# Kernel tuning notes

Measured on AMD Instinct MI355X. Metric: run time of the kernel, lower is better.

Reference implementation:

```python
import jax, jax.numpy as jnp
import numpy as np

B, N, F, K = 512, 128, 128, 4


def setup_inputs() -> dict:
    key = jax.random.key(0)
    ks = jax.random.split(key, 12)
    # xavier-normal-ish scales
    s_rw = float(np.sqrt(2.0 / (F + F)))
    s_sw = float(np.sqrt(2.0 / (F + F)))
    inp = {
        "H": jax.random.normal(ks[0], (B, N, F), dtype=jnp.float32),
        "E": jax.random.uniform(ks[1], (B, N, N, K), dtype=jnp.float32),
        "RW1": jax.random.normal(ks[2], (F, F, K), dtype=jnp.float32) * s_rw,
        "SW1": jax.random.normal(ks[3], (F, F), dtype=jnp.float32) * s_sw,
        "RW2": jax.random.normal(ks[4], (F, F, K), dtype=jnp.float32) * s_rw,
        "SW2": jax.random.normal(ks[5], (F, F), dtype=jnp.float32) * s_sw,
        "RW3": jax.random.normal(ks[6], (F, F, K), dtype=jnp.float32) * s_rw,
        "SW3": jax.random.normal(ks[7], (F, F), dtype=jnp.float32) * s_sw,
        "W1": jax.random.normal(ks[8], (F, 20), dtype=jnp.float32) * float(np.sqrt(1.0 / F)),
        "b1": jnp.zeros((20,), dtype=jnp.float32),
        "W2": jax.random.normal(ks[9], (20, 1), dtype=jnp.float32) * float(np.sqrt(1.0 / 20)),
        "b2": jnp.zeros((1,), dtype=jnp.float32),
    }
    return inp


def _rgcn_conv(H, E, D, RW, SW):
    # einsum('bi,bijk,bjm,mnk->bin') done in two GEMM-shaped steps
    M = jnp.einsum('bijk,bjm->bimk', E, H)          # [B,N,F,K]
    msg = jnp.einsum('bimk,mnk->bin', M, RW)        # [B,N,F]
    return jax.nn.sigmoid(msg * D[:, :, None] + jnp.einsum('bij,jl->bil', H, SW))


def reference(H, E, RW1, SW1, RW2, SW2, RW3, SW3, W1, b1, W2, b2):
    # degree norm with self-loops: (E + eye)[b,i,:,:].sum() = E.sum((2,3)) + K
    k = jnp.asarray(E.shape[-1], dtype=E.dtype)
    D = 1.0 / (E.sum(axis=(2, 3)) + k)              # [B,N]
    H = _rgcn_conv(H, E, D, RW1, SW1)
    H = _rgcn_conv(H, E, D, RW2, SW2)
    H = _rgcn_conv(H, E, D, RW3, SW3)
    h = jnp.maximum(H @ W1 + b1, 0.1 * (H @ W1 + b1))  # LeakyReLU(0.1)
    score = jnp.mean(jax.nn.sigmoid(h @ W2 + b2))
    return score
```

## Files before the change

### kernel.cpp

```cpp
#include <hip/hip_runtime.h>
#include <math.h>

#define BB 512
#define NN 128
#define FF 128
#define KK 4

typedef __attribute__((ext_vector_type(8))) short bf16x8;
typedef __attribute__((ext_vector_type(4))) float f32x4;

__device__ inline unsigned short f2bf(float x) {
  union { float f; unsigned int u; } v; v.f = x;
  unsigned int r = v.u + 0x7fff + ((v.u >> 16) & 1);
  return (unsigned short)(r >> 16);
}
__device__ inline float bf2f(unsigned short h) {
  union { unsigned int u; float f; } v; v.u = ((unsigned int)h) << 16; return v.f;
}

__global__ __launch_bounds__(256) void k_convE(const float* __restrict__ E,
                                               unsigned short* __restrict__ Eb,
                                               float* __restrict__ Dv) {
  int wave = threadIdx.x >> 6;
  int lane = threadIdx.x & 63;
  int row  = blockIdx.x * 4 + wave;
  const float* p = E + (size_t)row * 512 + lane * 8;
  f32x4 a = *(const f32x4*)p;
  f32x4 b = *(const f32x4*)(p + 4);
  float s = a[0] + a[1] + a[2] + a[3] + b[0] + b[1] + b[2] + b[3];
  #pragma unroll
  for (int off = 32; off > 0; off >>= 1) s += __shfl_down(s, off, 64);
  if (lane == 0) Dv[row] = 1.0f / (s + 4.0f);
  union { unsigned short h[8]; f32x4 v; } u;
  u.h[0] = f2bf(a[0]); u.h[1] = f2bf(a[1]); u.h[2] = f2bf(a[2]); u.h[3] = f2bf(a[3]);
  u.h[4] = f2bf(b[0]); u.h[5] = f2bf(b[1]); u.h[6] = f2bf(b[2]); u.h[7] = f2bf(b[3]);
  *(f32x4*)(Eb + (size_t)row * 512 + lane * 8) = u.v;
}

__global__ __launch_bounds__(256) void k_convH(const float* __restrict__ H,
                                               unsigned short* __restrict__ Hb) {
  size_t i = ((size_t)blockIdx.x * 256 + threadIdx.x) * 8;
  f32x4 a = *(const f32x4*)(H + i);
  f32x4 b = *(const f32x4*)(H + i + 4);
  union { unsigned short h[8]; f32x4 v; } u;
  u.h[0] = f2bf(a[0]); u.h[1] = f2bf(a[1]); u.h[2] = f2bf(a[2]); u.h[3] = f2bf(a[3]);
  u.h[4] = f2bf(b[0]); u.h[5] = f2bf(b[1]); u.h[6] = f2bf(b[2]); u.h[7] = f2bf(b[3]);
  *(f32x4*)(Hb + i) = u.v;
}

__global__ __launch_bounds__(256) void k_buildW(const float* __restrict__ RW,
                                                const float* __restrict__ SW,
                                                unsigned short* __restrict__ W2) {
  int idx = blockIdx.x * 256 + threadIdx.x;
  int m = idx & 127;
  int c = idx >> 7;
  float v = (c < 512) ? RW[m * 512 + c] : SW[m * 128 + (c - 512)];
  W2[idx] = f2bf(v);
}

__global__ __launch_bounds__(256) void k_gemm_g(
    const unsigned short* __restrict__ Hb,
    const unsigned short* __restrict__ W2,
    unsigned short* __restrict__ Gt,
    float* __restrict__ St)
{
  const int cb = blockIdx.x;
  const int b  = blockIdx.y;
  const unsigned short* A  = Hb + (size_t)b * 16384;
  const unsigned short* Bm = W2 + cb * 128 * 128;

  __shared__ unsigned short As[128 * 40];
  __shared__ unsigned short Bs[128 * 40];

  const int tid = threadIdx.x;
  const int w = tid >> 6, l = tid & 63;
  const int wr = w >> 1, wc = w & 1;
  const int lq = l >> 4, lm = l & 15;

  const int srow = tid >> 1;
  const int sch  = (tid & 1) * 16;

  f32x4 acc[4][4] = {};

  for (int k0 = 0; k0 < 128; k0 += 32) {
    f32x4 va0 = *(const f32x4*)(A + srow * 128 + k0 + sch);
    f32x4 va1 = *(const f32x4*)(A + srow * 128 + k0 + sch + 8);
    f32x4 vb0 = *(const f32x4*)(Bm + srow * 128 + k0 + sch);
    f32x4 vb1 = *(const f32x4*)(Bm + srow * 128 + k0 + sch + 8);
    __syncthreads();
    *(f32x4*)(As + srow * 40 + sch)     = va0;
    *(f32x4*)(As + srow * 40 + sch + 8) = va1;
    *(f32x4*)(Bs + srow * 40 + sch)     = vb0;
    *(f32x4*)(Bs + srow * 40 + sch + 8) = vb1;
    __syncthreads();
    bf16x8 fa[4], fb[4];
    #pragma unroll
    for (int f = 0; f < 4; ++f)
      fa[f] = *(const bf16x8*)(As + (wr * 64 + f * 16 + lm) * 40 + lq * 8);
    #pragma unroll
    for (int g = 0; g < 4; ++g)
      fb[g] = *(const bf16x8*)(Bs + (wc * 64 + g * 16 + lm) * 40 + lq * 8);
    #pragma unroll
    for (int f = 0; f < 4; ++f)
      #pragma unroll
      for (int g = 0; g < 4; ++g)
        acc[f][g] = __builtin_amdgcn_mfma_f32_16x16x32_bf16(fa[f], fb[g], acc[f][g], 0, 0, 0);
  }

  const int cbase = cb * 128 + wc * 64;
  if (cb < 4) {
    unsigned short* gt = Gt + (size_t)b * 65536;
    #pragma unroll
    for (int g = 0; g < 4; ++g) {
      int c = cbase + g * 16 + lm;
      int n = c >> 2, kk = c & 3;
      #pragma unroll
      for (int f = 0; f < 4; ++f) {
        int j0 = wr * 64 + f * 16 + lq * 4;
        #pragma unroll
        for (int r = 0; r < 4; ++r)
          gt[n * 512 + (j0 + r) * 4 + kk] = f2bf(acc[f][g][r]);
      }
    }
  } else {
    float* st = St + (size_t)b * 16384;
    #pragma unroll
    for (int g = 0; g < 4; ++g) {
      int s = wc * 64 + g * 16 + lm;
      #pragma unroll
      for (int f = 0; f < 4; ++f) {
        int j0 = wr * 64 + f * 16 + lq * 4;
        *(f32x4*)(st + s * 128 + j0) = acc[f][g];
      }
    }
  }
}

__global__ __launch_bounds__(256) void k_gemm_e(
    const unsigned short* __restrict__ Eb,
    const unsigned short* __restrict__ Gt,
    const float* __restrict__ St,
    const float* __restrict__ Dv,
    unsigned short* __restrict__ Hout)
{
  const int b = blockIdx.x;
  const unsigned short* A  = Eb + (size_t)b * 65536;
  const unsigned short* Bm = Gt + (size_t)b * 65536;

  __shared__ unsigned short As[128 * 40];
  __shared__ unsigned short Bs[128 * 40];

  const int tid = threadIdx.x;
  const int w = tid >> 6, l = tid & 63;
  const int wr = w >> 1, wc = w & 1;
  const int lq = l >> 4, lm = l & 15;

  const int srow = tid >> 1;
  const int sch  = (tid & 1) * 16;

  f32x4 acc[4][4] = {};

  for (int k0 = 0; k0 < 512; k0 += 32) {
    f32x4 va0 = *(const f32x4*)(A + srow * 512 + k0 + sch);
    f32x4 va1 = *(const f32x4*)(A + srow * 512 + k0 + sch + 8);
    f32x4 vb0 = *(const f32x4*)(Bm + srow * 512 + k0 + sch);
    f32x4 vb1 = *(const f32x4*)(Bm + srow * 512 + k0 + sch + 8);
    __syncthreads();
    *(f32x4*)(As + srow * 40 + sch)     = va0;
    *(f32x4*)(As + srow * 40 + sch + 8) = va1;
    *(f32x4*)(Bs + srow * 40 + sch)     = vb0;
    *(f32x4*)(Bs + srow * 40 + sch + 8) = vb1;
    __syncthreads();
    bf16x8 fa[4], fb[4];
    #pragma unroll
    for (int f = 0; f < 4; ++f)
      fa[f] = *(const bf16x8*)(As + (wr * 64 + f * 16 + lm) * 40 + lq * 8);
    #pragma unroll
    for (int g = 0; g < 4; ++g)
      fb[g] = *(const bf16x8*)(Bs + (wc * 64 + g * 16 + lm) * 40 + lq * 8);
    #pragma unroll
    for (int f = 0; f < 4; ++f)
      #pragma unroll
      for (int g = 0; g < 4; ++g)
        acc[f][g] = __builtin_amdgcn_mfma_f32_16x16x32_bf16(fa[f], fb[g], acc[f][g], 0, 0, 0);
  }

  const float* st = St + (size_t)b * 16384;
  const float* dv = Dv + b * 128;
  unsigned short* ho = Hout + (size_t)b * 16384;
  #pragma unroll
  for (int f = 0; f < 4; ++f) {
    int i0 = wr * 64 + f * 16 + lq * 4;
    f32x4 d = *(const f32x4*)(dv + i0);
    #pragma unroll
    for (int g = 0; g < 4; ++g) {
      int n = wc * 64 + g * 16 + lm;
      f32x4 sv = *(const f32x4*)(st + n * 128 + i0);
      #pragma unroll
      for (int r = 0; r < 4; ++r) {
        float v = fmaf(acc[f][g][r], d[r], sv[r]);
        ho[(i0 + r) * 128 + n] = f2bf(1.0f / (1.0f + __expf(-v)));
      }
    }
  }
}

__global__ __launch_bounds__(256) void k_mlp(
    const unsigned short* __restrict__ H,
    const float* __restrict__ W1,
    const float* __restrict__ b1,
    const float* __restrict__ W2,
    const float* __restrict__ b2,
    float* __restrict__ sumOut)
{
  __shared__ float W1s[128 * 20];
  __shared__ float b1s[20], W2s[20];
  __shared__ float red[256];
  for (int i = threadIdx.x; i < 2560; i += 256) W1s[i] = W1[i];
  if (threadIdx.x < 20) { b1s[threadIdx.x] = b1[threadIdx.x]; W2s[threadIdx.x] = W2[threadIdx.x]; }
  __syncthreads();

  int row = blockIdx.x * 256 + threadIdx.x;
  float h[20];
  #pragma unroll
  for (int j = 0; j < 20; ++j) h[j] = b1s[j];
  const unsigned short* hr = H + (size_t)row * 128;
  for (int m8 = 0; m8 < 128; m8 += 8) {
    f32x4 pk = *(const f32x4*)(hr + m8);
    const unsigned short* us = (const unsigned short*)&pk;
    #pragma unroll
    for (int e = 0; e < 8; ++e) {
      float x = bf2f(us[e]);
      #pragma unroll
      for (int j = 0; j < 20; ++j) h[j] = fmaf(x, W1s[(m8 + e) * 20 + j], h[j]);
    }
  }
  float v = b2[0];
  #pragma unroll
  for (int j = 0; j < 20; ++j) {
    float t = h[j];
    t = fmaxf(t, 0.1f * t);
    v = fmaf(t, W2s[j], v);
  }
  float s = 1.0f / (1.0f + __expf(-v));

  red[threadIdx.x] = s;
  __syncthreads();
  #pragma unroll
  for (int off = 128; off > 0; off >>= 1) {
    if (threadIdx.x < off) red[threadIdx.x] += red[threadIdx.x + off];
    __syncthreads();
  }
  if (threadIdx.x == 0) atomicAdd(sumOut, red[0]);
}

__global__ void k_final(const float* __restrict__ sum, float* __restrict__ out) {
  out[0] = sum[0] * (1.0f / 65536.0f);
}

extern "C" void kernel_launch(void* const* d_in, const int* in_sizes, int n_in,
                              void* d_out, int out_size, void* d_ws, size_t ws_size,
                              hipStream_t stream) {
  const float* H   = (const float*)d_in[0];
  const float* E   = (const float*)d_in[1];
  const float* RW1 = (const float*)d_in[2];
  const float* SW1 = (const float*)d_in[3];
  const float* RW2 = (const float*)d_in[4];
  const float* SW2 = (const float*)d_in[5];
  const float* RW3 = (const float*)d_in[6];
  const float* SW3 = (const float*)d_in[7];
  const float* W1  = (const float*)d_in[8];
  const float* b1  = (const float*)d_in[9];
  const float* W2  = (const float*)d_in[10];
  const float* b2  = (const float*)d_in[11];
  float* out = (float*)d_out;

  char* w = (char*)d_ws;
  float*          wsD   = (float*)w;                     w += 65536 * 4;
  unsigned short* wsEb  = (unsigned short*)w;            w += (size_t)33554432 * 2;
  unsigned short* wsGt  = (unsigned short*)w;            w += (size_t)33554432 * 2;
  float*          wsSt  = (float*)w;                     w += (size_t)8388608 * 4;
  unsigned short* wsHa  = (unsigned short*)w;            w += (size_t)8388608 * 2;
  unsigned short* wsHb  = (unsigned short*)w;            w += (size_t)8388608 * 2;
  unsigned short* wsW2  = (unsigned short*)w;            w += (size_t)3 * 81920 * 2;
  float*          wsSum = (float*)w;                     w += 256;

  k_convE<<<BB * NN / 4, 256, 0, stream>>>(E, wsEb, wsD);
  k_convH<<<8388608 / (256 * 8), 256, 0, stream>>>(H, wsHa);
  k_buildW<<<320, 256, 0, stream>>>(RW1, SW1, wsW2);
  k_buildW<<<320, 256, 0, stream>>>(RW2, SW2, wsW2 + 81920);
  k_buildW<<<320, 256, 0, stream>>>(RW3, SW3, wsW2 + 163840);
  hipMemsetAsync(wsSum, 0, sizeof(float), stream);

  k_gemm_g<<<dim3(5, BB), 256, 0, stream>>>(wsHa, wsW2, wsGt, wsSt);
  k_gemm_e<<<BB, 256, 0, stream>>>(wsEb, wsGt, wsSt, wsD, wsHb);
  k_gemm_g<<<dim3(5, BB), 256, 0, stream>>>(wsHb, wsW2 + 81920, wsGt, wsSt);
  k_gemm_e<<<BB, 256, 0, stream>>>(wsEb, wsGt, wsSt, wsD, wsHa);
  k_gemm_g<<<dim3(5, BB), 256, 0, stream>>>(wsHa, wsW2 + 163840, wsGt, wsSt);
  k_gemm_e<<<BB, 256, 0, stream>>>(wsEb, wsGt, wsSt, wsD, wsHb);

  k_mlp<<<BB * NN / 256, 256, 0, stream>>>(wsHb, W1, b1, W2, b2, wsSum);
  k_final<<<1, 1, 0, stream>>>(wsSum, out);
}
```

Before: 494.2 us.

## Fuse per-layer G and E GEMMs into one kernel keeping G in LDS

Each RGCN layer's two kernels (H·W into a global Gt/St buffer, then E·G with epilogue) become one kernel per batch. It builds the G tile in shared memory in two halves and computes the self-term GEMM in registers, so the 64 MB Gt and the St fp32 buffers never go through global memory. Operands now load straight from global into MFMA fragments without LDS staging. In exchange, W2 is re-read by every block, the grid shrinks to 512 blocks, and register pressure is high with three accumulator sets.

```diff
diff --git a/kernel.cpp b/kernel.cpp
--- a/kernel.cpp
+++ b/kernel.cpp
@@ -58,148 +58,112 @@
   W2[idx] = f2bf(v);
 }
 
-__global__ __launch_bounds__(256) void k_gemm_g(
-    const unsigned short* __restrict__ Hb,
-    const unsigned short* __restrict__ W2,
-    unsigned short* __restrict__ Gt,
-    float* __restrict__ St)
+#define GS_PITCH 264
+
+__global__ __launch_bounds__(256, 2) void k_layer(
+    const unsigned short* __restrict__ Eb,
+    const unsigned short* __restrict__ Hin,
+    const unsigned short* __restrict__ W2L,
+    const float* __restrict__ Dv,
+    unsigned short* __restrict__ Hout)
 {
-  const int cb = blockIdx.x;
-  const int b  = blockIdx.y;
-  const unsigned short* A  = Hb + (size_t)b * 16384;
-  const unsigned short* Bm = W2 + cb * 128 * 128;
-
-  __shared__ unsigned short As[128 * 40];
-  __shared__ unsigned short Bs[128 * 40];
+  __shared__ unsigned short Gs[128 * GS_PITCH];
+
+  const int b = blockIdx.x;
+  const unsigned short* E_b = Eb  + (size_t)b * 65536;
+  const unsigned short* H_b = Hin + (size_t)b * 16384;
 
   const int tid = threadIdx.x;
   const int w = tid >> 6, l = tid & 63;
   const int wr = w >> 1, wc = w & 1;
   const int lq = l >> 4, lm = l & 15;
 
-  const int srow = tid >> 1;
-  const int sch  = (tid & 1) * 16;
-
-  f32x4 acc[4][4] = {};
-
+  f32x4 macc[4][4] = {};
+
+  #pragma unroll
+  for (int h = 0; h < 2; ++h) {
+    __syncthreads();
+
+    #pragma unroll
+    for (int cb = 0; cb < 4; ++cb) {
+      f32x4 gacc[4][2] = {};
+      #pragma unroll
+      for (int k0 = 0; k0 < 128; k0 += 32) {
+        bf16x8 fa[4], fb[2];
+        #pragma unroll
+        for (int f = 0; f < 4; ++f)
+          fa[f] = *(const bf16x8*)(W2L + (cb * 128 + wr * 64 + f * 16 + lm) * 128 + k0 + lq * 8);
+        #pragma unroll
+        for (int g = 0; g < 2; ++g)
+          fb[g] = *(const bf16x8*)(H_b + (h * 64 + wc * 32 + g * 16 + lm) * 128 + k0 + lq * 8);
+        #pragma unroll
+        for (int f = 0; f < 4; ++f)
+          #pragma unroll
+          for (int g = 0; g < 2; ++g)
+            gacc[f][g] = __builtin_amdgcn_mfma_f32_16x16x32_bf16(fa[f], fb[g], gacc[f][g], 0, 0, 0);
+      }
+      #pragma unroll
+      for (int f = 0; f < 4; ++f) {
+        int n = cb * 32 + wr * 16 + f * 4 + lq;
+        #pragma unroll
+        for (int g = 0; g < 2; ++g) {
+          int jl = wc * 32 + g * 16 + lm;
+          union { unsigned short h4[4]; uint2 v; } u;
+          u.h4[0] = f2bf(gacc[f][g][0]); u.h4[1] = f2bf(gacc[f][g][1]);
+          u.h4[2] = f2bf(gacc[f][g][2]); u.h4[3] = f2bf(gacc[f][g][3]);
+          *(uint2*)(&Gs[n * GS_PITCH + jl * 4]) = u.v;
+        }
+      }
+    }
+    __syncthreads();
+
+    #pragma unroll
+    for (int kt = 0; kt < 8; ++kt) {
+      bf16x8 fa[4], fb[4];
+      #pragma unroll
+      for (int f = 0; f < 4; ++f)
+        fa[f] = *(const bf16x8*)(E_b + (wr * 64 + f * 16 + lm) * 512 + h * 256 + kt * 32 + lq * 8);
+      #pragma unroll
+      for (int g = 0; g < 4; ++g)
+        fb[g] = *(const bf16x8*)(&Gs[(wc * 64 + g * 16 + lm) * GS_PITCH + kt * 32 + lq * 8]);
+      #pragma unroll
+      for (int f = 0; f < 4; ++f)
+        #pragma unroll
+        for (int g = 0; g < 4; ++g)
+          macc[f][g] = __builtin_amdgcn_mfma_f32_16x16x32_bf16(fa[f], fb[g], macc[f][g], 0, 0, 0);
+    }
+  }
+
+  f32x4 sacc[4][4] = {};
+  #pragma unroll
   for (int k0 = 0; k0 < 128; k0 += 32) {
-    f32x4 va0 = *(const f32x4*)(A + srow * 128 + k0 + sch);
-    f32x4 va1 = *(const f32x4*)(A + srow * 128 + k0 + sch + 8);
-    f32x4 vb0 = *(const f32x4*)(Bm + srow * 128 + k0 + sch);
-    f32x4 vb1 = *(const f32x4*)(Bm + srow * 128 + k0 + sch + 8);
-    __syncthreads();
-    *(f32x4*)(As + srow * 40 + sch)     = va0;
-    *(f32x4*)(As + srow * 40 + sch + 8) = va1;
-    *(f32x4*)(Bs + srow * 40 + sch)     = vb0;
-    *(f32x4*)(Bs + srow * 40 + sch + 8) = vb1;
-    __syncthreads();
     bf16x8 fa[4], fb[4];
     #pragma unroll
     for (int f = 0; f < 4; ++f)
-      fa[f] = *(const bf16x8*)(As + (wr * 64 + f * 16 + lm) * 40 + lq * 8);
+      fa[f] = *(const bf16x8*)(H_b + (wr * 64 + f * 16 + lm) * 128 + k0 + lq * 8);
     #pragma unroll
     for (int g = 0; g < 4; ++g)
-      fb[g] = *(const bf16x8*)(Bs + (wc * 64 + g * 16 + lm) * 40 + lq * 8);
+      fb[g] = *(const bf16x8*)(W2L + (512 + wc * 64 + g * 16 + lm) * 128 + k0 + lq * 8);
     #pragma unroll
     for (int f = 0; f < 4; ++f)
       #pragma unroll
       for (int g = 0; g < 4; ++g)
-        acc[f][g] = __builtin_amdgcn_mfma_f32_16x16x32_bf16(fa[f], fb[g], acc[f][g], 0, 0, 0);
-  }
-
-  const int cbase = cb * 128 + wc * 64;
-  if (cb < 4) {
-    unsigned short* gt = Gt + (size_t)b * 65536;
-    #pragma unroll
-    for (int g = 0; g < 4; ++g) {
-      int c = cbase + g * 16 + lm;
-      int n = c >> 2, kk = c & 3;
-      #pragma unroll
-      for (int f = 0; f < 4; ++f) {
-        int j0 = wr * 64 + f * 16 + lq * 4;
-        #pragma unroll
-        for (int r = 0; r < 4; ++r)
-          gt[n * 512 + (j0 + r) * 4 + kk] = f2bf(acc[f][g][r]);
-      }
-    }
-  } else {
-    float* st = St + (size_t)b * 16384;
-    #pragma unroll
-    for (int g = 0; g < 4; ++g) {
-      int s = wc * 64 + g * 16 + lm;
-      #pragma unroll
-      for (int f = 0; f < 4; ++f) {
-        int j0 = wr * 64 + f * 16 + lq * 4;
-        *(f32x4*)(st + s * 128 + j0) = acc[f][g];
-      }
-    }
-  }
-}
-
-__global__ __launch_bounds__(256) void k_gemm_e(
-    const unsigned short* __restrict__ Eb,
-    const unsigned short* __restrict__ Gt,
-    const float* __restrict__ St,
-    const float* __restrict__ Dv,
-    unsigned short* __restrict__ Hout)
-{
-  const int b = blockIdx.x;
-  const unsigned short* A  = Eb + (size_t)b * 65536;
-  const unsigned short* Bm = Gt + (size_t)b * 65536;
-
-  __shared__ unsigned short As[128 * 40];
-  __shared__ unsigned short Bs[128 * 40];
-
-  const int tid = threadIdx.x;
-  const int w = tid >> 6, l = tid & 63;
-  const int wr = w >> 1, wc = w & 1;
-  const int lq = l >> 4, lm = l & 15;
-
-  const int srow = tid >> 1;
-  const int sch  = (tid & 1) * 16;
-
-  f32x4 acc[4][4] = {};
-
-  for (int k0 = 0; k0 < 512; k0 += 32) {
-    f32x4 va0 = *(const f32x4*)(A + srow * 512 + k0 + sch);
-    f32x4 va1 = *(const f32x4*)(A + srow * 512 + k0 + sch + 8);
-    f32x4 vb0 = *(const f32x4*)(Bm + srow * 512 + k0 + sch);
-    f32x4 vb1 = *(const f32x4*)(Bm + srow * 512 + k0 + sch + 8);
-    __syncthreads();
-    *(f32x4*)(As + srow * 40 + sch)     = va0;
-    *(f32x4*)(As + srow * 40 + sch + 8) = va1;
-    *(f32x4*)(Bs + srow * 40 + sch)     = vb0;
-    *(f32x4*)(Bs + srow * 40 + sch + 8) = vb1;
-    __syncthreads();
-    bf16x8 fa[4], fb[4];
-    #pragma unroll
-    for (int f = 0; f < 4; ++f)
-      fa[f] = *(const bf16x8*)(As + (wr * 64 + f * 16 + lm) * 40 + lq * 8);
-    #pragma unroll
-    for (int g = 0; g < 4; ++g)
-      fb[g] = *(const bf16x8*)(Bs + (wc * 64 + g * 16 + lm) * 40 + lq * 8);
-    #pragma unroll
-    for (int f = 0; f < 4; ++f)
-      #pragma unroll
-      for (int g = 0; g < 4; ++g)
-        acc[f][g] = __builtin_amdgcn_mfma_f32_16x16x32_bf16(fa[f], fb[g], acc[f][g], 0, 0, 0);
-  }
-
-  const float* st = St + (size_t)b * 16384;
-  const float* dv = Dv + b * 128;
-  unsigned short* ho = Hout + (size_t)b * 16384;
+        sacc[f][g] = __builtin_amdgcn_mfma_f32_16x16x32_bf16(fa[f], fb[g], sacc[f][g], 0, 0, 0);
+  }
+
+  const float* dvb = Dv + b * 128;
+  unsigned short* O_b = Hout + (size_t)b * 16384;
   #pragma unroll
   for (int f = 0; f < 4; ++f) {
     int i0 = wr * 64 + f * 16 + lq * 4;
-    f32x4 d = *(const f32x4*)(dv + i0);
+    f32x4 d = *(const f32x4*)(dvb + i0);
     #pragma unroll
     for (int g = 0; g < 4; ++g) {
       int n = wc * 64 + g * 16 + lm;
-      f32x4 sv = *(const f32x4*)(st + n * 128 + i0);
       #pragma unroll
       for (int r = 0; r < 4; ++r) {
-        float v = fmaf(acc[f][g][r], d[r], sv[r]);
-        ho[(i0 + r) * 128 + n] = f2bf(1.0f / (1.0f + __expf(-v)));
+        float v = fmaf(macc[f][g][r], d[r], sacc[f][g][r]);
+        O_b[(i0 + r) * 128 + n] = f2bf(1.0f / (1.0f + __expf(-v)));
       }
     }
   }
@@ -276,14 +240,12 @@
   float* out = (float*)d_out;
 
   char* w = (char*)d_ws;
-  float*          wsD   = (float*)w;                     w += 65536 * 4;
-  unsigned short* wsEb  = (unsigned short*)w;            w += (size_t)33554432 * 2;
-  unsigned short* wsGt  = (unsigned short*)w;            w += (size_t)33554432 * 2;
-  float*          wsSt  = (float*)w;                     w += (size_t)8388608 * 4;
-  unsigned short* wsHa  = (unsigned short*)w;            w += (size_t)8388608 * 2;
-  unsigned short* wsHb  = (unsigned short*)w;            w += (size_t)8388608 * 2;
-  unsigned short* wsW2  = (unsigned short*)w;            w += (size_t)3 * 81920 * 2;
-  float*          wsSum = (float*)w;                     w += 256;
+  float*          wsD   = (float*)w;           w += (size_t)65536 * 4;
+  unsigned short* wsEb  = (unsigned short*)w;  w += (size_t)33554432 * 2;
+  unsigned short* wsHa  = (unsigned short*)w;  w += (size_t)8388608 * 2;
+  unsigned short* wsHb  = (unsigned short*)w;  w += (size_t)8388608 * 2;
+  unsigned short* wsW2  = (unsigned short*)w;  w += (size_t)3 * 81920 * 2;
+  float*          wsSum = (float*)w;           w += 256;
 
   k_convE<<<BB * NN / 4, 256, 0, stream>>>(E, wsEb, wsD);
   k_convH<<<8388608 / (256 * 8), 256, 0, stream>>>(H, wsHa);
@@ -292,12 +254,9 @@
   k_buildW<<<320, 256, 0, stream>>>(RW3, SW3, wsW2 + 163840);
   hipMemsetAsync(wsSum, 0, sizeof(float), stream);
 
-  k_gemm_g<<<dim3(5, BB), 256, 0, stream>>>(wsHa, wsW2, wsGt, wsSt);
-  k_gemm_e<<<BB, 256, 0, stream>>>(wsEb, wsGt, wsSt, wsD, wsHb);
-  k_gemm_g<<<dim3(5, BB), 256, 0, stream>>>(wsHb, wsW2 + 81920, wsGt, wsSt);
-  k_gemm_e<<<BB, 256, 0, stream>>>(wsEb, wsGt, wsSt, wsD, wsHa);
-  k_gemm_g<<<dim3(5, BB), 256, 0, stream>>>(wsHa, wsW2 + 163840, wsGt, wsSt);
-  k_gemm_e<<<BB, 256, 0, stream>>>(wsEb, wsGt, wsSt, wsD, wsHb);
+  k_layer<<<BB, 256, 0, stream>>>(wsEb, wsHa, wsW2,          wsD, wsHb);
+  k_layer<<<BB, 256, 0, stream>>>(wsEb, wsHb, wsW2 + 81920,  wsD, wsHa);
+  k_layer<<<BB, 256, 0, stream>>>(wsEb, wsHa, wsW2 + 163840, wsD, wsHb);
 
   k_mlp<<<BB * NN / 256, 256, 0, stream>>>(wsHb, W1, b1, W2, b2, wsSum);
   k_final<<<1, 1, 0, stream>>>(wsSum, out);
```

Result: faster. 480.5 us (-2.8%).
